# Performance work log

Hardware: AMD Instinct MI355X
Metric: run time of the kernel (lower is better)

## Reference

```python
import jax, jax.numpy as jnp
import numpy as np

TOPK = 300
NUM_LEVELS = 3
GATE_TEMP = 1.0


def _normalized_grid(h, w):
    # matches torch: linspace(-1,1) meshgrid 'ij', stack (xx, yy) -> [h*w, 2]
    y = jnp.linspace(-1.0, 1.0, h, dtype=jnp.float32)
    x = jnp.linspace(-1.0, 1.0, w, dtype=jnp.float32)
    yy, xx = jnp.meshgrid(y, x, indexing='ij')
    return jnp.stack((xx, yy), axis=-1).reshape(h * w, 2)


def setup_inputs() -> dict:
    key = jax.random.key(0)
    ks = jax.random.split(key, 10)
    C, H_DIM, MAXL = 256, 256, 8
    shapes = [(8, C, 100, 152), (8, C, 50, 76), (8, C, 25, 38)]
    inp = {}
    for i, s in enumerate(shapes):
        inp[f'f{i}'] = jax.random.normal(ks[i], s, dtype=jnp.float32)
    inp['conv_w'] = jax.random.normal(ks[3], (C,), dtype=jnp.float32) * (1.0 / np.sqrt(C))
    inp['conv_b'] = jnp.zeros((1,), dtype=jnp.float32)
    inp['level_emb'] = jax.random.normal(ks[4], (MAXL, H_DIM), dtype=jnp.float32)
    qin = C + H_DIM + 3  # 515
    inp['w1'] = jax.random.normal(ks[5], (qin, H_DIM), dtype=jnp.float32) * (1.0 / np.sqrt(qin))
    inp['b1'] = jnp.zeros((H_DIM,), dtype=jnp.float32)
    inp['w2'] = jax.random.normal(ks[6], (H_DIM, H_DIM), dtype=jnp.float32) * (1.0 / np.sqrt(H_DIM))
    inp['b2'] = jnp.zeros((H_DIM,), dtype=jnp.float32)
    inp['gate_w'] = jax.random.normal(ks[7], (H_DIM, MAXL), dtype=jnp.float32) * (1.0 / np.sqrt(H_DIM))
    inp['gate_b'] = jnp.zeros((MAXL,), dtype=jnp.float32)
    inp['residual_scale'] = jnp.zeros((1,), dtype=jnp.float32)  # residual_scale_init=0.0
    return inp


def reference(f0, f1, f2, conv_w, conv_b, level_emb, w1, b1, w2, b2, gate_w, gate_b, residual_scale):
    levels = [f0, f1, f2]
    B = f0.shape[0]
    tok_s, tok_f, tok_p, tok_l = [], [], [], []
    for i, f in enumerate(levels):
        _, C, H, W = f.shape
        # 1x1 conv proxy objectness score -> [B, H*W]
        s = jnp.einsum('bchw,c->bhw', f, conv_w).reshape(B, H * W) + conv_b[0]
        tok_s.append(s)
        tok_f.append(f.reshape(B, C, H * W).transpose(0, 2, 1))       # [B, HW, C]
        tok_p.append(jnp.broadcast_to(_normalized_grid(H, W), (B, H * W, 2)))
        tok_l.append(jnp.full((B, H * W), i, dtype=jnp.int32))
    scores = jnp.concatenate(tok_s, axis=1)   # [B, N]
    feats = jnp.concatenate(tok_f, axis=1)    # [B, N, C]
    pos = jnp.concatenate(tok_p, axis=1)      # [B, N, 2]
    lvl = jnp.concatenate(tok_l, axis=1)      # [B, N]

    top_vals, top_idx = jax.lax.top_k(scores, TOPK)                     # [B, K]
    fk = jnp.take_along_axis(feats, top_idx[:, :, None], axis=1)        # [B, K, C]
    pk = jnp.take_along_axis(pos, top_idx[:, :, None], axis=1)          # [B, K, 2]
    lk = jnp.take_along_axis(lvl, top_idx, axis=1)                      # [B, K]
    sp = jax.nn.sigmoid(top_vals)                                       # [B, K]

    q = jnp.concatenate([fk, level_emb[lk], pk, sp[..., None]], axis=-1)  # [B, K, C+H+3]
    h = jax.nn.relu(q @ w1 + b1)
    h = jax.nn.relu(h @ w2 + b2)
    logits = (h @ gate_w + gate_b)[..., :NUM_LEVELS]                     # [B, K, L]
    gates = jax.nn.softmax(logits / GATE_TEMP, axis=-1)
    alpha = gates.mean(axis=1)                                           # [B, L]
    scale = 1.0 + residual_scale[0] * alpha                              # [B, L]

    outs = [f * scale[:, i][:, None, None, None] for i, f in enumerate(levels)]
    # flatten the output feature dict into one [B, sum(C*H*W)] array
    return jnp.concatenate([o.reshape(B, -1) for o in outs], axis=1)
```

## Files before the change

### kernel.cpp

```cpp
#include <hip/hip_runtime.h>
#include <hip/hip_bf16.h>

#define NTOK 19950
#define NTOKP 19968
#define KTOP 300
#define NB 8
#define NQ 2400
#define QDIM 520
#define NCC 8

typedef float f32x4 __attribute__((ext_vector_type(4)));

__device__ __forceinline__ uint32_t fkey(float f) {
    uint32_t u = __float_as_uint(f);
    return (u & 0x80000000u) ? ~u : (u | 0x80000000u);
}

__global__ __launch_bounds__(256) void score_part_kernel(
    const float* __restrict__ f0, const float* __restrict__ f1, const float* __restrict__ f2,
    const float* __restrict__ conv_w, float* __restrict__ partial)
{
    __shared__ float cwch[32];
    const int tid = threadIdx.x;
    const int blk = blockIdx.x;
    int b, cc;
    if (blk < 256)      { b = blk >> 5; cc = (blk >> 2) & 7; }
    else if (blk < 320) { int i = blk - 256; b = i >> 3; cc = i & 7; }
    else                { int i = blk - 320; b = i >> 3; cc = i & 7; }
    if (tid < 32) cwch[tid] = conv_w[cc * 32 + tid];
    __syncthreads();

    if (blk < 256) {
        const int q = blk & 3;
        const f32x4* b4 = (const f32x4*)(f0 + ((size_t)(b * 256 + cc * 32)) * 15200) + q * 950;
        const int s3 = (tid + 768 < 950) ? tid + 768 : 0;
        f32x4 a0 = {0,0,0,0}, a1 = a0, a2 = a0, a3 = a0;
        #pragma unroll 4
        for (int c = 0; c < 32; ++c) {
            const f32x4* r = b4 + (size_t)c * 3800;
            const float w = cwch[c];
            f32x4 v0 = r[tid], v1 = r[tid + 256], v2 = r[tid + 512], v3 = r[s3];
            a0 += v0 * w; a1 += v1 * w; a2 += v2 * w; a3 += v3 * w;
        }
        f32x4* o4 = (f32x4*)(partial + (size_t)(cc * NB + b) * NTOKP) + q * 950;
        o4[tid] = a0; o4[tid + 256] = a1; o4[tid + 512] = a2;
        if (tid + 768 < 950) o4[tid + 768] = a3;
    } else if (blk < 320) {
        const f32x4* b4 = (const f32x4*)(f1 + ((size_t)(b * 256 + cc * 32)) * 3800);
        const int s3 = (tid + 768 < 950) ? tid + 768 : 0;
        f32x4 a0 = {0,0,0,0}, a1 = a0, a2 = a0, a3 = a0;
        #pragma unroll 4
        for (int c = 0; c < 32; ++c) {
            const f32x4* r = b4 + (size_t)c * 950;
            const float w = cwch[c];
            f32x4 v0 = r[tid], v1 = r[tid + 256], v2 = r[tid + 512], v3 = r[s3];
            a0 += v0 * w; a1 += v1 * w; a2 += v2 * w; a3 += v3 * w;
        }
        f32x4* o4 = (f32x4*)(partial + (size_t)(cc * NB + b) * NTOKP + 15200);
        o4[tid] = a0; o4[tid + 256] = a1; o4[tid + 512] = a2;
        if (tid + 768 < 950) o4[tid + 768] = a3;
    } else {
        const float2* b2 = (const float2*)(f2 + ((size_t)(b * 256 + cc * 32)) * 950);
        const int s1 = (tid + 256 < 475) ? tid + 256 : 0;
        float2 a0 = {0,0}, a1 = a0;
        #pragma unroll 4
        for (int c = 0; c < 32; ++c) {
            const float2* r = b2 + (size_t)c * 475;
            const float w = cwch[c];
            float2 v0 = r[tid], v1 = r[s1];
            a0.x += v0.x * w; a0.y += v0.y * w;
            a1.x += v1.x * w; a1.y += v1.y * w;
        }
        float2* o2 = (float2*)(partial + (size_t)(cc * NB + b) * NTOKP + 19000);
        if (tid < 475) o2[tid] = a0;
        if (tid + 256 < 475) o2[tid + 256] = a1;
    }
}

__global__ __launch_bounds__(256) void score_reduce_kernel(
    const float* __restrict__ partial, const float* __restrict__ conv_b,
    float* __restrict__ scores)
{
    const int t = blockIdx.x * 256 + threadIdx.x;
    if (t >= NB * NTOK) return;
    const int b = t / NTOK;
    const int i = t - b * NTOK;
    float s = 0.0f;
    #pragma unroll
    for (int cc = 0; cc < NCC; ++cc)
        s += partial[(size_t)(cc * NB + b) * NTOKP + i];
    scores[t] = s + conv_b[0];
}

__global__ __launch_bounds__(1024, 1) void topk_kernel(
    const float* __restrict__ scores, int* __restrict__ top_idx)
{
    __shared__ uint32_t key[NTOK];
    __shared__ int whist[16][256];
    __shared__ int suffix[257];
    __shared__ uint32_t s_prefix;
    __shared__ int s_Kr, s_cnt, s_tcnt;
    __shared__ int tie[1024];
    const int tid = threadIdx.x;
    const int wv = tid >> 6;
    const int b = blockIdx.x;
    const float* srow = scores + b * NTOK;
    for (int i = tid; i < NTOK; i += 1024) key[i] = fkey(srow[i]);
    if (tid == 0) { s_prefix = 0u; s_Kr = KTOP; suffix[256] = 0; }
    __syncthreads();
    uint32_t pmask = 0u;
    for (int pass = 0; pass < 4; ++pass) {
        const int shift = 24 - 8 * pass;
        for (int i = tid; i < 16 * 256; i += 1024) ((int*)whist)[i] = 0;
        __syncthreads();
        const uint32_t prefix = s_prefix;
        const int Kr = s_Kr;
        for (int i = tid; i < NTOK; i += 1024) {
            uint32_t k = key[i];
            if ((k & pmask) == prefix) atomicAdd(&whist[wv][(k >> shift) & 255], 1);
        }
        __syncthreads();
        if (tid < 256) {
            int s = 0;
            #pragma unroll
            for (int w = 0; w < 16; ++w) s += whist[w][tid];
            suffix[tid] = s;
        }
        __syncthreads();
        if (tid < 64) {
            const int c0 = suffix[tid * 4], c1 = suffix[tid * 4 + 1];
            const int c2 = suffix[tid * 4 + 2], c3 = suffix[tid * 4 + 3];
            const int tot = c0 + c1 + c2 + c3;
            int s = tot;
            #pragma unroll
            for (int off = 1; off < 64; off <<= 1) {
                int o = __shfl_down(s, off);
                if (tid + off < 64) s += o;
            }
            const int Sn = s - tot;
            suffix[tid * 4 + 3] = c3 + Sn;
            suffix[tid * 4 + 2] = c2 + c3 + Sn;
            suffix[tid * 4 + 1] = c1 + c2 + c3 + Sn;
            suffix[tid * 4 + 0] = tot + Sn;
        }
        __syncthreads();
        if (tid < 256) {
            int sgeq = suffix[tid];
            int sgt  = suffix[tid + 1];
            if (sgeq >= Kr && sgt < Kr) {
                s_prefix = prefix | ((uint32_t)tid << shift);
                s_Kr = Kr - sgt;
            }
        }
        __syncthreads();
        pmask |= (0xFFu << shift);
    }
    const uint32_t T = s_prefix;
    const int need = s_Kr;
    if (tid == 0) { s_cnt = 0; s_tcnt = 0; }
    __syncthreads();
    for (int i = tid; i < NTOK; i += 1024) {
        uint32_t k = key[i];
        if (k > T) {
            int p = atomicAdd(&s_cnt, 1);
            top_idx[b * KTOP + p] = i;
        } else if (k == T) {
            int p = atomicAdd(&s_tcnt, 1);
            if (p < 1024) tie[p] = i;
        }
    }
    __syncthreads();
    if (tid == 0) {
        int base = s_cnt;
        int tcnt = s_tcnt > 1024 ? 1024 : s_tcnt;
        for (int s = 0; s < need; ++s) {
            int mi = s;
            for (int u = s + 1; u < tcnt; ++u) if (tie[u] < tie[mi]) mi = u;
            int tmp = tie[s]; tie[s] = tie[mi]; tie[mi] = tmp;
            top_idx[b * KTOP + base + s] = tie[s];
        }
    }
}

#define QT 8
__global__ __launch_bounds__(512, 1) void mlp_kernel(
    const float* __restrict__ f0, const float* __restrict__ f1, const float* __restrict__ f2,
    const float* __restrict__ scores, const int* __restrict__ top_idx,
    const float* __restrict__ level_emb,
    const float* __restrict__ w1, const float* __restrict__ b1,
    const float* __restrict__ w2, const float* __restrict__ b2,
    const float* __restrict__ gate_w, const float* __restrict__ gate_b,
    float* __restrict__ G)
{
    __shared__ __align__(16) float q[QT][QDIM];
    __shared__ __align__(16) float part[QT][256];
    __shared__ __align__(16) float h[QT][256];
    __shared__ int s_b[QT], s_lvl[QT], s_hw[QT], s_HW[QT];
    const int tid = threadIdx.x;
    const int out = tid & 255;
    const int kh = tid >> 8;
    const int k0 = blockIdx.x * QT;

    if (tid < QT) {
        const int kk = k0 + tid;
        const int bq = kk / KTOP;
        const int idx = top_idx[kk];
        int lvl, hw, HWl, Wl, Hl;
        if (idx < 15200)      { lvl = 0; hw = idx;         HWl = 15200; Wl = 152; Hl = 100; }
        else if (idx < 19000) { lvl = 1; hw = idx - 15200; HWl = 3800;  Wl = 76;  Hl = 50;  }
        else                  { lvl = 2; hw = idx - 19000; HWl = 950;   Wl = 38;  Hl = 25;  }
        s_b[tid] = bq; s_lvl[tid] = lvl; s_hw[tid] = hw; s_HW[tid] = HWl;
        int hh = hw / Wl, ww = hw - hh * Wl;
        float x = -1.0f + 2.0f * (float)ww / (float)(Wl - 1);
        float y = -1.0f + 2.0f * (float)hh / (float)(Hl - 1);
        float sv = scores[bq * NTOK + idx];
        float sp = 1.0f / (1.0f + expf(-sv));
        q[tid][512] = x; q[tid][513] = y; q[tid][514] = sp;
        q[tid][515] = 0.0f; q[tid][516] = 0.0f; q[tid][517] = 0.0f;
        q[tid][518] = 0.0f; q[tid][519] = 0.0f;
    }
    __syncthreads();
    #pragma unroll
    for (int j = tid; j < QT * 256; j += 512) {
        const int t = j >> 8, c = j & 255;
        const int lvl = s_lvl[t];
        const float* f = (lvl == 0) ? f0 : ((lvl == 1) ? f1 : f2);
        q[t][c]       = f[((size_t)(s_b[t] * 256 + c)) * s_HW[t] + s_hw[t]];
        q[t][256 + c] = level_emb[lvl * 256 + c];
    }
    __syncthreads();

    float acc[QT];

    {
        #pragma unroll
        for (int t = 0; t < QT; ++t) acc[t] = 0.0f;
        const float* wp = w1 + (size_t)(kh * 256) * 256 + out;
        float a0 = wp[0], a1 = wp[256], a2 = wp[512], a3 = wp[768];
        for (int i4 = 0; i4 < 64; ++i4) {
            float c0 = a0, c1 = a1, c2 = a2, c3 = a3;
            const float* wn = wp + 1024;
            if (i4 < 63) { a0 = wn[0]; a1 = wn[256]; a2 = wn[512]; a3 = wn[768]; }
            wp = wn;
            const int kb = kh * 256 + i4 * 4;
            #pragma unroll
            for (int t = 0; t < QT; ++t) {
                float4 qv = *reinterpret_cast<const float4*>(&q[t][kb]);
                acc[t] += qv.x * c0 + qv.y * c1 + qv.z * c2 + qv.w * c3;
            }
        }
        if (kh) {
            for (int r = 512; r < 515; ++r) {
                float wv = w1[(size_t)r * 256 + out];
                #pragma unroll
                for (int t = 0; t < QT; ++t) acc[t] += q[t][r] * wv;
            }
            #pragma unroll
            for (int t = 0; t < QT; ++t) part[t][out] = acc[t];
        }
    }
    __syncthreads();
    if (kh == 0) {
        float bj = b1[out];
        #pragma unroll
        for (int t = 0; t < QT; ++t) h[t][out] = fmaxf(acc[t] + part[t][out] + bj, 0.0f);
    }
    __syncthreads();

    {
        #pragma unroll
        for (int t = 0; t < QT; ++t) acc[t] = 0.0f;
        const float* wp = w2 + (size_t)(kh * 128) * 256 + out;
        float a0 = wp[0], a1 = wp[256], a2 = wp[512], a3 = wp[768];
        for (int i4 = 0; i4 < 32; ++i4) {
            float c0 = a0, c1 = a1, c2 = a2, c3 = a3;
            const float* wn = wp + 1024;
            if (i4 < 31) { a0 = wn[0]; a1 = wn[256]; a2 = wn[512]; a3 = wn[768]; }
            wp = wn;
            const int kb = kh * 128 + i4 * 4;
            #pragma unroll
            for (int t = 0; t < QT; ++t) {
                float4 hv = *reinterpret_cast<const float4*>(&h[t][kb]);
                acc[t] += hv.x * c0 + hv.y * c1 + hv.z * c2 + hv.w * c3;
            }
        }
        if (kh) {
            #pragma unroll
            for (int t = 0; t < QT; ++t) part[t][out] = acc[t];
        }
    }
    __syncthreads();
    if (kh == 0) {
        float bj = b2[out];
        #pragma unroll
        for (int t = 0; t < QT; ++t) q[t][out] = fmaxf(acc[t] + part[t][out] + bj, 0.0f);
    }
    __syncthreads();

    if (tid < 256) {
        const int t = tid >> 5, seg = tid & 31;
        float l0 = 0.f, l1 = 0.f, l2 = 0.f;
        for (int c = seg * 8; c < seg * 8 + 8; ++c) {
            float hv = q[t][c];
            l0 += hv * gate_w[c * 8 + 0];
            l1 += hv * gate_w[c * 8 + 1];
            l2 += hv * gate_w[c * 8 + 2];
        }
        float* gp = &part[0][0];
        gp[(t * 32 + seg) * 3 + 0] = l0;
        gp[(t * 32 + seg) * 3 + 1] = l1;
        gp[(t * 32 + seg) * 3 + 2] = l2;
    }
    __syncthreads();
    if (tid < QT) {
        const int t = tid;
        float l0 = gate_b[0], l1 = gate_b[1], l2 = gate_b[2];
        const float* gp = &part[0][0];
        for (int seg = 0; seg < 32; ++seg) {
            l0 += gp[(t * 32 + seg) * 3 + 0];
            l1 += gp[(t * 32 + seg) * 3 + 1];
            l2 += gp[(t * 32 + seg) * 3 + 2];
        }
        float m = fmaxf(l0, fmaxf(l1, l2));
        float e0 = expf(l0 - m), e1 = expf(l1 - m), e2 = expf(l2 - m);
        float inv = 1.0f / (e0 + e1 + e2);
        G[(k0 + t) * 3 + 0] = e0 * inv;
        G[(k0 + t) * 3 + 1] = e1 * inv;
        G[(k0 + t) * 3 + 2] = e2 * inv;
    }
}

__global__ __launch_bounds__(256) void out_kernel(
    const f32x4* __restrict__ f0, const f32x4* __restrict__ f1, const f32x4* __restrict__ f2,
    const float* __restrict__ G, const float* __restrict__ rs, f32x4* __restrict__ out)
{
    __shared__ float red[3][32];
    __shared__ float ssc[3];
    const int b = blockIdx.y;
    const int tid = threadIdx.x;
    if (tid < 96) {
        const int l = tid / 32, c = tid % 32;
        float s = 0.0f;
        const int kb = c * 10;
        const int ke = (kb + 10 < KTOP) ? kb + 10 : KTOP;
        for (int k = kb; k < ke; ++k) s += G[(size_t)(b * KTOP + k) * 3 + l];
        red[l][c] = s;
    }
    __syncthreads();
    for (int off = 16; off > 0; off >>= 1) {
        if (tid < 96) {
            const int l = tid / 32, c = tid % 32;
            if (c < off) red[l][c] += red[l][c + off];
        }
        __syncthreads();
    }
    if (tid < 3) ssc[tid] = 1.0f + rs[0] * (red[tid][0] / (float)KTOP);
    __syncthreads();

    const int t0 = blockIdx.x * 256 + tid;
    const int TPB = gridDim.x * 256;
    f32x4* ob = out + (size_t)b * 1276800;
    {
        const float sc = ssc[0];
        const f32x4* src = f0 + (size_t)b * 972800;
        for (int r = t0; r < 972800; r += TPB)
            __builtin_nontemporal_store(src[r] * sc, &ob[r]);
    }
    {
        const float sc = ssc[1];
        const f32x4* src = f1 + (size_t)b * 243200;
        f32x4* o1 = ob + 972800;
        for (int r = t0; r < 243200; r += TPB)
            __builtin_nontemporal_store(src[r] * sc, &o1[r]);
    }
    {
        const float sc = ssc[2];
        const f32x4* src = f2 + (size_t)b * 60800;
        f32x4* o2 = ob + 1216000;
        for (int r = t0; r < 60800; r += TPB)
            __builtin_nontemporal_store(src[r] * sc, &o2[r]);
    }
}

extern "C" void kernel_launch(void* const* d_in, const int* in_sizes, int n_in,
                              void* d_out, int out_size, void* d_ws, size_t ws_size,
                              hipStream_t stream)
{
    const float* f0        = (const float*)d_in[0];
    const float* f1        = (const float*)d_in[1];
    const float* f2        = (const float*)d_in[2];
    const float* conv_w    = (const float*)d_in[3];
    const float* conv_b    = (const float*)d_in[4];
    const float* level_emb = (const float*)d_in[5];
    const float* w1        = (const float*)d_in[6];
    const float* b1        = (const float*)d_in[7];
    const float* w2        = (const float*)d_in[8];
    const float* b2        = (const float*)d_in[9];
    const float* gate_w    = (const float*)d_in[10];
    const float* gate_b    = (const float*)d_in[11];
    const float* rs        = (const float*)d_in[12];

    char* ws = (char*)d_ws;
    float* scores  = (float*)ws;
    int*   top_idx = (int*)(ws + 640 * 1024);
    float* G       = (float*)(ws + 656 * 1024);
    float* partial = (float*)(ws + 704 * 1024);

    score_part_kernel<<<384, 256, 0, stream>>>(f0, f1, f2, conv_w, partial);
    score_reduce_kernel<<<(NB * NTOK + 255) / 256, 256, 0, stream>>>(partial, conv_b, scores);
    topk_kernel<<<NB, 1024, 0, stream>>>(scores, top_idx);
    mlp_kernel<<<NQ / QT, 512, 0, stream>>>(f0, f1, f2, scores, top_idx, level_emb,
                                            w1, b1, w2, b2, gate_w, gate_b, G);
    out_kernel<<<dim3(256, NB), 256, 0, stream>>>((const f32x4*)f0, (const f32x4*)f1,
                                                  (const f32x4*)f2, G, rs, (f32x4*)d_out);
}
```

Before: 156.8 us.

## Split score channels finer and fuse first radix-select histogram into score reduce

```diff
diff --git a/kernel.cpp b/kernel.cpp
--- a/kernel.cpp
+++ b/kernel.cpp
@@ -7,7 +7,7 @@
 #define NB 8
 #define NQ 2400
 #define QDIM 520
-#define NCC 8
+#define NCC 16
 
 typedef float f32x4 __attribute__((ext_vector_type(4)));
 
@@ -18,25 +18,27 @@
 
 __global__ __launch_bounds__(256) void score_part_kernel(
     const float* __restrict__ f0, const float* __restrict__ f1, const float* __restrict__ f2,
-    const float* __restrict__ conv_w, float* __restrict__ partial)
-{
-    __shared__ float cwch[32];
+    const float* __restrict__ conv_w, float* __restrict__ partial, int* __restrict__ ghist)
+{
+    __shared__ float cwch[16];
     const int tid = threadIdx.x;
     const int blk = blockIdx.x;
     int b, cc;
-    if (blk < 256)      { b = blk >> 5; cc = (blk >> 2) & 7; }
-    else if (blk < 320) { int i = blk - 256; b = i >> 3; cc = i & 7; }
-    else                { int i = blk - 320; b = i >> 3; cc = i & 7; }
-    if (tid < 32) cwch[tid] = conv_w[cc * 32 + tid];
-    __syncthreads();
-
-    if (blk < 256) {
+    if (blk < 512)      { b = blk >> 6; cc = (blk >> 2) & 15; }
+    else if (blk < 640) { int i = blk - 512; b = i >> 4; cc = i & 15; }
+    else                { int i = blk - 640; b = i >> 4; cc = i & 15; }
+    if (blk >= 640 && ((blk - 640) & 15) == 0 && tid < 256)
+        ghist[((blk - 640) >> 4) * 256 + tid] = 0;
+    if (tid < 16) cwch[tid] = conv_w[cc * 16 + tid];
+    __syncthreads();
+
+    if (blk < 512) {
         const int q = blk & 3;
-        const f32x4* b4 = (const f32x4*)(f0 + ((size_t)(b * 256 + cc * 32)) * 15200) + q * 950;
+        const f32x4* b4 = (const f32x4*)(f0 + ((size_t)(b * 256 + cc * 16)) * 15200) + q * 950;
         const int s3 = (tid + 768 < 950) ? tid + 768 : 0;
         f32x4 a0 = {0,0,0,0}, a1 = a0, a2 = a0, a3 = a0;
         #pragma unroll 4
-        for (int c = 0; c < 32; ++c) {
+        for (int c = 0; c < 16; ++c) {
             const f32x4* r = b4 + (size_t)c * 3800;
             const float w = cwch[c];
             f32x4 v0 = r[tid], v1 = r[tid + 256], v2 = r[tid + 512], v3 = r[s3];
@@ -45,12 +47,12 @@
         f32x4* o4 = (f32x4*)(partial + (size_t)(cc * NB + b) * NTOKP) + q * 950;
         o4[tid] = a0; o4[tid + 256] = a1; o4[tid + 512] = a2;
         if (tid + 768 < 950) o4[tid + 768] = a3;
-    } else if (blk < 320) {
-        const f32x4* b4 = (const f32x4*)(f1 + ((size_t)(b * 256 + cc * 32)) * 3800);
+    } else if (blk < 640) {
+        const f32x4* b4 = (const f32x4*)(f1 + ((size_t)(b * 256 + cc * 16)) * 3800);
         const int s3 = (tid + 768 < 950) ? tid + 768 : 0;
         f32x4 a0 = {0,0,0,0}, a1 = a0, a2 = a0, a3 = a0;
         #pragma unroll 4
-        for (int c = 0; c < 32; ++c) {
+        for (int c = 0; c < 16; ++c) {
             const f32x4* r = b4 + (size_t)c * 950;
             const float w = cwch[c];
             f32x4 v0 = r[tid], v1 = r[tid + 256], v2 = r[tid + 512], v3 = r[s3];
@@ -60,11 +62,11 @@
         o4[tid] = a0; o4[tid + 256] = a1; o4[tid + 512] = a2;
         if (tid + 768 < 950) o4[tid + 768] = a3;
     } else {
-        const float2* b2 = (const float2*)(f2 + ((size_t)(b * 256 + cc * 32)) * 950);
+        const float2* b2 = (const float2*)(f2 + ((size_t)(b * 256 + cc * 16)) * 950);
         const int s1 = (tid + 256 < 475) ? tid + 256 : 0;
         float2 a0 = {0,0}, a1 = a0;
         #pragma unroll 4
-        for (int c = 0; c < 32; ++c) {
+        for (int c = 0; c < 16; ++c) {
             const float2* r = b2 + (size_t)c * 475;
             const float w = cwch[c];
             float2 v0 = r[tid], v1 = r[s1];
@@ -72,28 +74,37 @@
             a1.x += v1.x * w; a1.y += v1.y * w;
         }
         float2* o2 = (float2*)(partial + (size_t)(cc * NB + b) * NTOKP + 19000);
-        if (tid < 475) o2[tid] = a0;
+        o2[tid] = a0;
         if (tid + 256 < 475) o2[tid + 256] = a1;
     }
 }
 
 __global__ __launch_bounds__(256) void score_reduce_kernel(
     const float* __restrict__ partial, const float* __restrict__ conv_b,
-    float* __restrict__ scores)
-{
-    const int t = blockIdx.x * 256 + threadIdx.x;
-    if (t >= NB * NTOK) return;
-    const int b = t / NTOK;
-    const int i = t - b * NTOK;
-    float s = 0.0f;
-    #pragma unroll
-    for (int cc = 0; cc < NCC; ++cc)
-        s += partial[(size_t)(cc * NB + b) * NTOKP + i];
-    scores[t] = s + conv_b[0];
+    float* __restrict__ scores, int* __restrict__ ghist)
+{
+    __shared__ int lh[256];
+    const int tid = threadIdx.x;
+    const int b = blockIdx.y;
+    const int i = blockIdx.x * 256 + tid;
+    lh[tid] = 0;
+    __syncthreads();
+    if (i < NTOK) {
+        float s = 0.0f;
+        #pragma unroll
+        for (int cc = 0; cc < NCC; ++cc)
+            s += partial[(size_t)(cc * NB + b) * NTOKP + i];
+        s += conv_b[0];
+        scores[b * NTOK + i] = s;
+        atomicAdd(&lh[fkey(s) >> 24], 1);
+    }
+    __syncthreads();
+    if (lh[tid]) atomicAdd(&ghist[b * 256 + tid], lh[tid]);
 }
 
 __global__ __launch_bounds__(1024, 1) void topk_kernel(
-    const float* __restrict__ scores, int* __restrict__ top_idx)
+    const float* __restrict__ scores, const int* __restrict__ ghist,
+    int* __restrict__ top_idx)
 {
     __shared__ uint32_t key[NTOK];
     __shared__ int whist[16][256];
@@ -106,10 +117,37 @@
     const int b = blockIdx.x;
     const float* srow = scores + b * NTOK;
     for (int i = tid; i < NTOK; i += 1024) key[i] = fkey(srow[i]);
-    if (tid == 0) { s_prefix = 0u; s_Kr = KTOP; suffix[256] = 0; }
-    __syncthreads();
-    uint32_t pmask = 0u;
-    for (int pass = 0; pass < 4; ++pass) {
+    if (tid == 0) { s_Kr = KTOP; suffix[256] = 0; }
+    if (tid < 256) suffix[tid] = ghist[b * 256 + tid];
+    __syncthreads();
+    if (tid < 64) {
+        const int c0 = suffix[tid * 4], c1 = suffix[tid * 4 + 1];
+        const int c2 = suffix[tid * 4 + 2], c3 = suffix[tid * 4 + 3];
+        const int tot = c0 + c1 + c2 + c3;
+        int s = tot;
+        #pragma unroll
+        for (int off = 1; off < 64; off <<= 1) {
+            int o = __shfl_down(s, off);
+            if (tid + off < 64) s += o;
+        }
+        const int Sn = s - tot;
+        suffix[tid * 4 + 3] = c3 + Sn;
+        suffix[tid * 4 + 2] = c2 + c3 + Sn;
+        suffix[tid * 4 + 1] = c1 + c2 + c3 + Sn;
+        suffix[tid * 4 + 0] = tot + Sn;
+    }
+    __syncthreads();
+    if (tid < 256) {
+        int sgeq = suffix[tid];
+        int sgt  = suffix[tid + 1];
+        if (sgeq >= KTOP && sgt < KTOP) {
+            s_prefix = (uint32_t)tid << 24;
+            s_Kr = KTOP - sgt;
+        }
+    }
+    __syncthreads();
+    uint32_t pmask = 0xFF000000u;
+    for (int pass = 1; pass < 4; ++pass) {
         const int shift = 24 - 8 * pass;
         for (int i = tid; i < 16 * 256; i += 1024) ((int*)whist)[i] = 0;
         __syncthreads();
@@ -404,11 +442,12 @@
     float* scores  = (float*)ws;
     int*   top_idx = (int*)(ws + 640 * 1024);
     float* G       = (float*)(ws + 656 * 1024);
+    int*   ghist   = (int*)(ws + 688 * 1024);
     float* partial = (float*)(ws + 704 * 1024);
 
-    score_part_kernel<<<384, 256, 0, stream>>>(f0, f1, f2, conv_w, partial);
-    score_reduce_kernel<<<(NB * NTOK + 255) / 256, 256, 0, stream>>>(partial, conv_b, scores);
-    topk_kernel<<<NB, 1024, 0, stream>>>(scores, top_idx);
+    score_part_kernel<<<768, 256, 0, stream>>>(f0, f1, f2, conv_w, partial, ghist);
+    score_reduce_kernel<<<dim3(78, NB), 256, 0, stream>>>(partial, conv_b, scores, ghist);
+    topk_kernel<<<NB, 1024, 0, stream>>>(scores, ghist, top_idx);
     mlp_kernel<<<NQ / QT, 512, 0, stream>>>(f0, f1, f2, scores, top_idx, level_emb,
                                             w1, b1, w2, b2, gate_w, gate_b, G);
     out_kernel<<<dim3(256, NB), 256, 0, stream>>>((const f32x4*)f0, (const f32x4*)f1,
```

Result: faster. 150.2 us (-4.2%).
